# Performance work log

Measured on AMD Instinct MI355X. Metric: run time of the kernel, lower is better.

The kernel has to match this reference:

```python
import jax, jax.numpy as jnp
import numpy as np

D_EMB = 1024
D_HEAD = 64
B = 4
T = 4096


def setup_inputs() -> dict:
    key = jax.random.key(0)
    kx, kk, kq, kv = jax.random.split(key, 4)
    s = 1.0 / np.sqrt(D_EMB)  # torch Linear default init scale (uniform bound)
    x = jax.random.normal(kx, (B, T, D_EMB), dtype=jnp.float32)
    Wk = jax.random.uniform(kk, (D_HEAD, D_EMB), jnp.float32, -s, s)
    Wq = jax.random.uniform(kq, (D_HEAD, D_EMB), jnp.float32, -s, s)
    Wv = jax.random.uniform(kv, (D_HEAD, D_EMB), jnp.float32, -s, s)
    return {"x": x, "Wk": Wk, "Wq": Wq, "Wv": Wv}


def reference(x, Wk, Wq, Wv):
    # x: (B, T, d_emb); W*: (d_head, d_emb) -- torch Linear stores (out, in)
    k = jnp.einsum('bte,he->bth', x, Wk)
    q = jnp.einsum('bte,he->bth', x, Wq)
    v = jnp.einsum('bte,he->bth', x, Wv)
    scale = D_HEAD ** (-0.5)
    a = jnp.einsum('bth,bsh->bts', q, k) * scale  # (B, T, T)
    Tlen = x.shape[-2]
    causal = jnp.tril(jnp.ones((Tlen, Tlen), dtype=bool))
    a = jnp.where(causal, a, -jnp.inf)
    a = jax.nn.softmax(a, axis=-1)
    return jnp.einsum('bts,bsh->bth', a, v)  # (B, T, d_head)
```

## Files before the change

### kernel.cpp

```cpp
#include <hip/hip_runtime.h>
#include <hip/hip_bf16.h>

#define D_EMB 1024
#define T_LEN 4096
#define NTASK 576

typedef short short8 __attribute__((ext_vector_type(8)));
typedef float f32x4 __attribute__((ext_vector_type(4)));
typedef float f32x16 __attribute__((ext_vector_type(16)));
typedef float float4v __attribute__((ext_vector_type(4)));

__device__ __forceinline__ unsigned short f32_to_bf16(float f) {
    union { float f; unsigned int u; } c; c.f = f;
    unsigned int u = c.u;
    return (unsigned short)((u + 0x7FFFu + ((u >> 16) & 1u)) >> 16);
}
__device__ __forceinline__ float bf16_to_f32(unsigned short v) {
    union { unsigned int u; float f; } c; c.u = ((unsigned int)v) << 16;
    return c.f;
}
__device__ __forceinline__ unsigned cvtpk_bf16(float a, float b) {
    unsigned r;
    asm("v_cvt_pk_bf16_f32 %0, %1, %2" : "=v"(r) : "v"(a), "v"(b));
    return r;
}
__device__ __forceinline__ void gl_lds16(const void* g, void* l) {
    __builtin_amdgcn_global_load_lds(
        (const __attribute__((address_space(1))) unsigned int*)(g),
        (__attribute__((address_space(3))) unsigned int*)(l), 16, 0, 0);
}

#define QSCALE (0.125f * 1.44269504f)

__global__ __launch_bounds__(256) void convert_w(const float* __restrict__ Wk,
                                                 const float* __restrict__ Wq,
                                                 const float* __restrict__ Wv,
                                                 unsigned short* __restrict__ Wb) {
    int e = (blockIdx.x * 256 + threadIdx.x) * 8;
    const float* src;
    if (e < 65536) src = Wk + e;
    else if (e < 131072) src = Wq + (e - 65536);
    else src = Wv + (e - 131072);
    float4v a0 = *(const float4v*)src;
    float4v a1 = *(const float4v*)(src + 4);
    short8 r;
    r[0] = (short)f32_to_bf16(a0[0]); r[1] = (short)f32_to_bf16(a0[1]);
    r[2] = (short)f32_to_bf16(a0[2]); r[3] = (short)f32_to_bf16(a0[3]);
    r[4] = (short)f32_to_bf16(a1[0]); r[5] = (short)f32_to_bf16(a1[1]);
    r[6] = (short)f32_to_bf16(a1[2]); r[7] = (short)f32_to_bf16(a1[3]);
    int row = e >> 10;
    int dst = e ^ ((row & 7) << 3);
    *(short8*)(Wb + dst) = r;
}

__global__ __launch_bounds__(256, 2) void qkv_proj(const float* __restrict__ x,
                                                   const unsigned short* __restrict__ Wb,
                                                   unsigned short* __restrict__ Kb,
                                                   unsigned short* __restrict__ Qb,
                                                   unsigned short* __restrict__ Vt) {
    __shared__ __attribute__((aligned(16))) unsigned short Wsl[2][12288];

    int tid = threadIdx.x;
    int lane = tid & 63, wave = tid >> 6;
    int lo = lane & 15, hi = lane >> 4;
    int rg = wave >> 1, nh = wave & 1;
    int row0 = blockIdx.x * 32;

    const float* xp = x + (size_t)(row0 + rg * 16 + lo) * D_EMB + hi * 8;

    f32x4 acc[6];
#pragma unroll
    for (int i = 0; i < 6; i++) acc[i] = (f32x4){0.f, 0.f, 0.f, 0.f};

    float4v xa0 = *(const float4v*)(xp);
    float4v xa1 = *(const float4v*)(xp + 4);
    float4v xa2 = *(const float4v*)(xp + 32);
    float4v xa3 = *(const float4v*)(xp + 36);

#pragma unroll
    for (int j = 0; j < 6; j++) {
        int unit = j * 4 + wave;
        int u = unit * 64 + lane;
        gl_lds16(Wb + (size_t)(u >> 3) * D_EMB + (u & 7) * 8, &Wsl[0][unit * 512]);
    }
    __syncthreads();

    int buf = 0;
    int xorm = (lo & 7) << 4;
    int rowbase = nh * 96 + lo;

    for (int kt = 0; kt < 16; kt++) {
        int ktn = (kt < 15) ? kt + 1 : 15;
        const float* pn = xp + ktn * 64;
        float4v xn0 = *(const float4v*)(pn);
        float4v xn1 = *(const float4v*)(pn + 4);
        float4v xn2 = *(const float4v*)(pn + 32);
        float4v xn3 = *(const float4v*)(pn + 36);

        if (kt < 15) {
            int k0n = (kt + 1) * 64;
#pragma unroll
            for (int j = 0; j < 6; j++) {
                int unit = j * 4 + wave;
                int u = unit * 64 + lane;
                gl_lds16(Wb + (size_t)(u >> 3) * D_EMB + k0n + (u & 7) * 8,
                         &Wsl[buf ^ 1][unit * 512]);
            }
        }

        short8 af[2];
        {
            union { unsigned u[4]; short8 s; } c;
            c.u[0] = cvtpk_bf16(xa0[0], xa0[1]);
            c.u[1] = cvtpk_bf16(xa0[2], xa0[3]);
            c.u[2] = cvtpk_bf16(xa1[0], xa1[1]);
            c.u[3] = cvtpk_bf16(xa1[2], xa1[3]);
            af[0] = c.s;
            c.u[0] = cvtpk_bf16(xa2[0], xa2[1]);
            c.u[1] = cvtpk_bf16(xa2[2], xa2[3]);
            c.u[2] = cvtpk_bf16(xa3[0], xa3[1]);
            c.u[3] = cvtpk_bf16(xa3[2], xa3[3]);
            af[1] = c.s;
        }

        const char* sb = (const char*)&Wsl[buf][0];
#pragma unroll
        for (int i = 0; i < 6; i++) {
            int row = rowbase + i * 16;
#pragma unroll
            for (int ks = 0; ks < 2; ks++) {
                short8 bfrag = *(const short8*)(sb + row * 128 + ((ks * 64 + hi * 16) ^ xorm));
                acc[i] = __builtin_amdgcn_mfma_f32_16x16x32_bf16(af[ks], bfrag, acc[i], 0, 0, 0);
            }
        }
        __syncthreads();
        buf ^= 1;
        xa0 = xn0; xa1 = xn1; xa2 = xn2; xa3 = xn3;
    }

#pragma unroll
    for (int i = 0; i < 6; i++) {
        int n = nh * 6 + i;
#pragma unroll
        for (int r = 0; r < 4; r++) {
            int grow = row0 + rg * 16 + hi * 4 + r;
            float val = acc[i][r];
            if (n < 4) {
                Kb[(size_t)grow * 64 + n * 16 + lo] = f32_to_bf16(val);
            } else if (n < 8) {
                Qb[(size_t)grow * 64 + (n - 4) * 16 + lo] = f32_to_bf16(val * QSCALE);
            } else {
                int bb = grow >> 12;
                Vt[((size_t)bb * 64 + (n - 8) * 16 + lo) * T_LEN + (grow & 4095)] = f32_to_bf16(val);
            }
        }
    }
}

__global__ __launch_bounds__(64, 3) void attn(const unsigned short* __restrict__ Qb,
                                              const unsigned short* __restrict__ Kb,
                                              const unsigned short* __restrict__ Vt,
                                              unsigned short* __restrict__ Opart,
                                              float* __restrict__ Mpart,
                                              float* __restrict__ Lpart) {
    int lane = threadIdx.x;
    int q32 = lane & 31;
    int hi = lane >> 5;
    int s = blockIdx.x;
    int b = blockIdx.y;

    int k = 7, rem = s;
    while (rem >= 16 * (k + 1)) { rem -= 16 * (k + 1); k--; }
    int cpt = k + 1;
    int ti = rem / cpt;
    int t = (k << 4) + 15 - ti;
    int c = rem - ti * cpt;

    int u0 = c * 16;
    int u1 = min(u0 + 16, t + 1);

    size_t base = (size_t)b * T_LEN;
    int q0 = t * 32;
    int qg = q0 + q32;

    short8 qf[4];
    const unsigned short* qp = Qb + (base + qg) * 64 + hi * 8;
#pragma unroll
    for (int d = 0; d < 4; d++) qf[d] = *(const short8*)(qp + d * 16);

    size_t vbase = ((size_t)b * 64 + q32) * T_LEN;
    f32x16 o0 = {0.f}, o1 = {0.f};
    float m = -3e38f, l = 0.f;

    short8 kc0, kc1, kc2, kc3, vc0, vc1, vc2, vc3;
    {
        const unsigned short* kp = Kb + (base + u0 * 32 + q32) * 64 + hi * 8;
        kc0 = *(const short8*)kp;
        kc1 = *(const short8*)(kp + 16);
        kc2 = *(const short8*)(kp + 32);
        kc3 = *(const short8*)(kp + 48);
        const unsigned short* vp = Vt + vbase + u0 * 32 + hi * 8;
        vc0 = *(const short8*)vp;
        vc1 = *(const short8*)(vp + 16);
        vc2 = *(const short8*)(vp + 32 * T_LEN);
        vc3 = *(const short8*)(vp + 32 * T_LEN + 16);
    }

    for (int u = u0; u < u1; ++u) {
        int un = (u + 1 < u1) ? u + 1 : u;
        const unsigned short* kpn = Kb + (base + un * 32 + q32) * 64 + hi * 8;
        short8 kn0 = *(const short8*)kpn;
        short8 kn1 = *(const short8*)(kpn + 16);
        short8 kn2 = *(const short8*)(kpn + 32);
        short8 kn3 = *(const short8*)(kpn + 48);
        const unsigned short* vpn = Vt + vbase + un * 32 + hi * 8;
        short8 vn0 = *(const short8*)vpn;
        short8 vn1 = *(const short8*)(vpn + 16);
        short8 vn2 = *(const short8*)(vpn + 32 * T_LEN);
        short8 vn3 = *(const short8*)(vpn + 32 * T_LEN + 16);

        f32x16 sc = {0.f};
        sc = __builtin_amdgcn_mfma_f32_32x32x16_bf16(kc0, qf[0], sc, 0, 0, 0);
        sc = __builtin_amdgcn_mfma_f32_32x32x16_bf16(kc1, qf[1], sc, 0, 0, 0);
        sc = __builtin_amdgcn_mfma_f32_32x32x16_bf16(kc2, qf[2], sc, 0, 0, 0);
        sc = __builtin_amdgcn_mfma_f32_32x32x16_bf16(kc3, qf[3], sc, 0, 0, 0);

        if (u == t) {
#pragma unroll
            for (int r = 0; r < 16; ++r) {
                int ko = (r & 3) + 8 * (r >> 2) + 4 * hi;
                sc[r] = (ko <= q32) ? sc[r] : -3e38f;
            }
        }

        float x0 = fmaxf(sc[0], sc[8]),  x1 = fmaxf(sc[1], sc[9]);
        float x2 = fmaxf(sc[2], sc[10]), x3 = fmaxf(sc[3], sc[11]);
        float x4 = fmaxf(sc[4], sc[12]), x5 = fmaxf(sc[5], sc[13]);
        float x6 = fmaxf(sc[6], sc[14]), x7 = fmaxf(sc[7], sc[15]);
        x0 = fmaxf(x0, x4); x1 = fmaxf(x1, x5); x2 = fmaxf(x2, x6); x3 = fmaxf(x3, x7);
        x0 = fmaxf(x0, x2); x1 = fmaxf(x1, x3);
        float mx = fmaxf(x0, x1);
        mx = fmaxf(mx, __shfl_xor(mx, 32));

        if (__any(mx > m + 8.0f)) {
            float mn = fmaxf(m, mx);
            float al = exp2f(m - mn);
            m = mn; l *= al;
#pragma unroll
            for (int r = 0; r < 16; ++r) { o0[r] *= al; o1[r] *= al; }
        }

#pragma unroll
        for (int r = 0; r < 16; ++r) sc[r] = exp2f(sc[r] - m);
        float y0 = (sc[0] + sc[8]) + (sc[4] + sc[12]);
        float y1 = (sc[1] + sc[9]) + (sc[5] + sc[13]);
        float y2 = (sc[2] + sc[10]) + (sc[6] + sc[14]);
        float y3 = (sc[3] + sc[11]) + (sc[7] + sc[15]);
        float sum = (y0 + y1) + (y2 + y3);
        sum += __shfl_xor(sum, 32);
        l += sum;

        unsigned bb0, bb1, bb2, bb3, bb4, bb5, bb6, bb7;
        asm("v_cvt_pk_bf16_f32 %0, %1, %2" : "=v"(bb0) : "v"(sc[0]),  "v"(sc[1]));
        asm("v_cvt_pk_bf16_f32 %0, %1, %2" : "=v"(bb1) : "v"(sc[2]),  "v"(sc[3]));
        asm("v_cvt_pk_bf16_f32 %0, %1, %2" : "=v"(bb2) : "v"(sc[4]),  "v"(sc[5]));
        asm("v_cvt_pk_bf16_f32 %0, %1, %2" : "=v"(bb3) : "v"(sc[6]),  "v"(sc[7]));
        asm("v_cvt_pk_bf16_f32 %0, %1, %2" : "=v"(bb4) : "v"(sc[8]),  "v"(sc[9]));
        asm("v_cvt_pk_bf16_f32 %0, %1, %2" : "=v"(bb5) : "v"(sc[10]), "v"(sc[11]));
        asm("v_cvt_pk_bf16_f32 %0, %1, %2" : "=v"(bb6) : "v"(sc[12]), "v"(sc[13]));
        asm("v_cvt_pk_bf16_f32 %0, %1, %2" : "=v"(bb7) : "v"(sc[14]), "v"(sc[15]));
        asm("v_permlane32_swap_b32 %0, %1" : "+v"(bb0), "+v"(bb2));
        asm("v_permlane32_swap_b32 %0, %1" : "+v"(bb1), "+v"(bb3));
        asm("v_permlane32_swap_b32 %0, %1" : "+v"(bb4), "+v"(bb6));
        asm("v_permlane32_swap_b32 %0, %1" : "+v"(bb5), "+v"(bb7));
        union U8 { unsigned u[4]; short8 s; };
        U8 p0; p0.u[0] = bb0; p0.u[1] = bb1; p0.u[2] = bb2; p0.u[3] = bb3;
        U8 p1; p1.u[0] = bb4; p1.u[1] = bb5; p1.u[2] = bb6; p1.u[3] = bb7;

        o0 = __builtin_amdgcn_mfma_f32_32x32x16_bf16(vc0, p0.s, o0, 0, 0, 0);
        o0 = __builtin_amdgcn_mfma_f32_32x32x16_bf16(vc1, p1.s, o0, 0, 0, 0);
        o1 = __builtin_amdgcn_mfma_f32_32x32x16_bf16(vc2, p0.s, o1, 0, 0, 0);
        o1 = __builtin_amdgcn_mfma_f32_32x32x16_bf16(vc3, p1.s, o1, 0, 0, 0);

        kc0 = kn0; kc1 = kn1; kc2 = kn2; kc3 = kn3;
        vc0 = vn0; vc1 = vn1; vc2 = vn2; vc3 = vn3;
    }

    size_t tbase = ((size_t)(b * NTASK + s) * 32 + q32) * 64;
#pragma unroll
    for (int hb = 0; hb < 2; hb++) {
#pragma unroll
        for (int g = 0; g < 4; g++) {
            float e0 = hb ? o1[4 * g] : o0[4 * g];
            float e1 = hb ? o1[4 * g + 1] : o0[4 * g + 1];
            float e2 = hb ? o1[4 * g + 2] : o0[4 * g + 2];
            float e3 = hb ? o1[4 * g + 3] : o0[4 * g + 3];
            unsigned w0, w1;
            asm("v_cvt_pk_bf16_f32 %0, %1, %2" : "=v"(w0) : "v"(e0), "v"(e1));
            asm("v_cvt_pk_bf16_f32 %0, %1, %2" : "=v"(w1) : "v"(e2), "v"(e3));
            int h0 = hb * 32 + g * 8 + hi * 4;
            *reinterpret_cast<uint2*>(Opart + tbase + h0) = make_uint2(w0, w1);
        }
    }
    if (lane < 32) {
        Mpart[(b * NTASK + s) * 32 + q32] = m;
        Lpart[(b * NTASK + s) * 32 + q32] = l;
    }
}

__global__ __launch_bounds__(256) void attn_merge(const unsigned short* __restrict__ Opart,
                                                  const float* __restrict__ Mpart,
                                                  const float* __restrict__ Lpart,
                                                  float* __restrict__ out) {
    int tid = threadIdx.x;
    int g = blockIdx.x * 64 + (tid >> 2);
    int h0 = (tid & 3) * 16;
    int b = g >> 12, t = g & 4095;
    int tile = t >> 5, r32 = t & 31;
    int k = tile >> 4;
    int nch = k + 1;
    int s0 = 16 * (36 - (((k + 1) * (k + 2)) >> 1)) + (15 - (tile & 15)) * nch;
    int tb = b * NTASK + s0;

    float mm = -3e38f;
    for (int i = 0; i < nch; i++) mm = fmaxf(mm, Mpart[(tb + i) * 32 + r32]);
    float ll = 0.f;
    float acc[16];
#pragma unroll
    for (int e = 0; e < 16; e++) acc[e] = 0.f;
    for (int i = 0; i < nch; i++) {
        float a = exp2f(Mpart[(tb + i) * 32 + r32] - mm);
        ll += a * Lpart[(tb + i) * 32 + r32];
        const unsigned short* op = Opart + ((size_t)(tb + i) * 32 + r32) * 64 + h0;
        short8 v0 = *(const short8*)op;
        short8 v1 = *(const short8*)(op + 8);
#pragma unroll
        for (int e = 0; e < 8; e++) {
            acc[e]     += a * bf16_to_f32((unsigned short)v0[e]);
            acc[8 + e] += a * bf16_to_f32((unsigned short)v1[e]);
        }
    }
    float inv = 1.f / ll;
    float* dst = out + (size_t)g * 64 + h0;
#pragma unroll
    for (int e = 0; e < 16; e++) dst[e] = acc[e] * inv;
}

extern "C" void kernel_launch(void* const* d_in, const int* in_sizes, int n_in,
                              void* d_out, int out_size, void* d_ws, size_t ws_size,
                              hipStream_t stream) {
    (void)in_sizes; (void)n_in; (void)out_size; (void)ws_size;
    const float* x  = (const float*)d_in[0];
    const float* Wk = (const float*)d_in[1];
    const float* Wq = (const float*)d_in[2];
    const float* Wv = (const float*)d_in[3];
    float* out = (float*)d_out;

    unsigned short* Wb = (unsigned short*)d_ws;
    unsigned short* Kb = Wb + 196608;
    unsigned short* Qb = Kb + 1048576;
    unsigned short* Vt = Qb + 1048576;
    unsigned short* Opart = Vt + 1048576;
    float* Mpart = (float*)(Opart + (size_t)4 * NTASK * 32 * 64);
    float* Lpart = Mpart + 4 * NTASK * 32;

    hipLaunchKernelGGL(convert_w, dim3(96), dim3(256), 0, stream, Wk, Wq, Wv, Wb);
    hipLaunchKernelGGL(qkv_proj, dim3(512), dim3(256), 0, stream, x, Wb, Kb, Qb, Vt);
    hipLaunchKernelGGL(attn, dim3(NTASK, 4), dim3(64), 0, stream, Qb, Kb, Vt, Opart, Mpart, Lpart);
    hipLaunchKernelGGL(attn_merge, dim3(256), dim3(256), 0, stream, Opart, Mpart, Lpart, out);
}
```

Before: 83.80 us.

## Halve attention chunk size and software-pipeline QK^T one step ahead

The causal split-K attention tasks now cover 8 key tiles instead of 16, which nearly doubles the task count (NTASK 576 to 1088) and gives finer load balance and more parallelism. The merge kernel's index math is updated to match. Inside the attention loop, the QK^T MFMAs for the next key tile are issued before the current tile's softmax and PV step, with K and V loads staggered, so matrix work overlaps with softmax. The projection kernel prefetches x two k-steps ahead. The cost is more partial outputs to write and merge, plus higher register pressure.

```diff
diff --git a/kernel.cpp b/kernel.cpp
--- a/kernel.cpp
+++ b/kernel.cpp
@@ -3,7 +3,7 @@
 
 #define D_EMB 1024
 #define T_LEN 4096
-#define NTASK 576
+#define NTASK 1088
 
 typedef short short8 __attribute__((ext_vector_type(8)));
 typedef float f32x4 __attribute__((ext_vector_type(4)));
@@ -76,6 +76,10 @@
     float4v xa1 = *(const float4v*)(xp + 4);
     float4v xa2 = *(const float4v*)(xp + 32);
     float4v xa3 = *(const float4v*)(xp + 36);
+    float4v xb0 = *(const float4v*)(xp + 64);
+    float4v xb1 = *(const float4v*)(xp + 68);
+    float4v xb2 = *(const float4v*)(xp + 96);
+    float4v xb3 = *(const float4v*)(xp + 100);
 
 #pragma unroll
     for (int j = 0; j < 6; j++) {
@@ -90,12 +94,12 @@
     int rowbase = nh * 96 + lo;
 
     for (int kt = 0; kt < 16; kt++) {
-        int ktn = (kt < 15) ? kt + 1 : 15;
+        int ktn = (kt < 14) ? kt + 2 : 15;
         const float* pn = xp + ktn * 64;
-        float4v xn0 = *(const float4v*)(pn);
-        float4v xn1 = *(const float4v*)(pn + 4);
-        float4v xn2 = *(const float4v*)(pn + 32);
-        float4v xn3 = *(const float4v*)(pn + 36);
+        float4v xc0 = *(const float4v*)(pn);
+        float4v xc1 = *(const float4v*)(pn + 4);
+        float4v xc2 = *(const float4v*)(pn + 32);
+        float4v xc3 = *(const float4v*)(pn + 36);
 
         if (kt < 15) {
             int k0n = (kt + 1) * 64;
@@ -135,7 +139,8 @@
         }
         __syncthreads();
         buf ^= 1;
-        xa0 = xn0; xa1 = xn1; xa2 = xn2; xa3 = xn3;
+        xa0 = xb0; xa1 = xb1; xa2 = xb2; xa3 = xb3;
+        xb0 = xc0; xb1 = xc1; xb2 = xc2; xb3 = xc3;
     }
 
 #pragma unroll
@@ -169,19 +174,18 @@
     int s = blockIdx.x;
     int b = blockIdx.y;
 
-    int k = 7, rem = s;
-    while (rem >= 16 * (k + 1)) { rem -= 16 * (k + 1); k--; }
+    int k = 15, rem = s;
+    while (rem >= 8 * (k + 1)) { rem -= 8 * (k + 1); k--; }
     int cpt = k + 1;
     int ti = rem / cpt;
-    int t = (k << 4) + 15 - ti;
+    int t = (k << 3) + 7 - ti;
     int c = rem - ti * cpt;
 
-    int u0 = c * 16;
-    int u1 = min(u0 + 16, t + 1);
+    int u0 = c * 8;
+    int u1 = min(u0 + 8, t + 1);
 
     size_t base = (size_t)b * T_LEN;
-    int q0 = t * 32;
-    int qg = q0 + q32;
+    int qg = t * 32 + q32;
 
     short8 qf[4];
     const unsigned short* qp = Qb + (base + qg) * 64 + hi * 8;
@@ -192,51 +196,61 @@
     f32x16 o0 = {0.f}, o1 = {0.f};
     float m = -3e38f, l = 0.f;
 
-    short8 kc0, kc1, kc2, kc3, vc0, vc1, vc2, vc3;
+    short8 kB0, kB1, kB2, kB3, vA0, vA1, vA2, vA3;
     {
         const unsigned short* kp = Kb + (base + u0 * 32 + q32) * 64 + hi * 8;
-        kc0 = *(const short8*)kp;
-        kc1 = *(const short8*)(kp + 16);
-        kc2 = *(const short8*)(kp + 32);
-        kc3 = *(const short8*)(kp + 48);
+        kB0 = *(const short8*)kp;
+        kB1 = *(const short8*)(kp + 16);
+        kB2 = *(const short8*)(kp + 32);
+        kB3 = *(const short8*)(kp + 48);
+    }
+    f32x16 scC = {0.f};
+    scC = __builtin_amdgcn_mfma_f32_32x32x16_bf16(kB0, qf[0], scC, 0, 0, 0);
+    scC = __builtin_amdgcn_mfma_f32_32x32x16_bf16(kB1, qf[1], scC, 0, 0, 0);
+    scC = __builtin_amdgcn_mfma_f32_32x32x16_bf16(kB2, qf[2], scC, 0, 0, 0);
+    scC = __builtin_amdgcn_mfma_f32_32x32x16_bf16(kB3, qf[3], scC, 0, 0, 0);
+    {
         const unsigned short* vp = Vt + vbase + u0 * 32 + hi * 8;
-        vc0 = *(const short8*)vp;
-        vc1 = *(const short8*)(vp + 16);
-        vc2 = *(const short8*)(vp + 32 * T_LEN);
-        vc3 = *(const short8*)(vp + 32 * T_LEN + 16);
+        vA0 = *(const short8*)vp;
+        vA1 = *(const short8*)(vp + 16);
+        vA2 = *(const short8*)(vp + 32 * T_LEN);
+        vA3 = *(const short8*)(vp + 32 * T_LEN + 16);
+        int un = (u0 + 1 < u1) ? u0 + 1 : u0;
+        const unsigned short* kp = Kb + (base + un * 32 + q32) * 64 + hi * 8;
+        kB0 = *(const short8*)kp;
+        kB1 = *(const short8*)(kp + 16);
+        kB2 = *(const short8*)(kp + 32);
+        kB3 = *(const short8*)(kp + 48);
     }
 
     for (int u = u0; u < u1; ++u) {
-        int un = (u + 1 < u1) ? u + 1 : u;
-        const unsigned short* kpn = Kb + (base + un * 32 + q32) * 64 + hi * 8;
-        short8 kn0 = *(const short8*)kpn;
-        short8 kn1 = *(const short8*)(kpn + 16);
-        short8 kn2 = *(const short8*)(kpn + 32);
-        short8 kn3 = *(const short8*)(kpn + 48);
-        const unsigned short* vpn = Vt + vbase + un * 32 + hi * 8;
-        short8 vn0 = *(const short8*)vpn;
-        short8 vn1 = *(const short8*)(vpn + 16);
-        short8 vn2 = *(const short8*)(vpn + 32 * T_LEN);
-        short8 vn3 = *(const short8*)(vpn + 32 * T_LEN + 16);
-
-        f32x16 sc = {0.f};
-        sc = __builtin_amdgcn_mfma_f32_32x32x16_bf16(kc0, qf[0], sc, 0, 0, 0);
-        sc = __builtin_amdgcn_mfma_f32_32x32x16_bf16(kc1, qf[1], sc, 0, 0, 0);
-        sc = __builtin_amdgcn_mfma_f32_32x32x16_bf16(kc2, qf[2], sc, 0, 0, 0);
-        sc = __builtin_amdgcn_mfma_f32_32x32x16_bf16(kc3, qf[3], sc, 0, 0, 0);
+        bool hn = (u + 1 < u1);
+        f32x16 scN = {0.f};
+        if (hn) {
+            scN = __builtin_amdgcn_mfma_f32_32x32x16_bf16(kB0, qf[0], scN, 0, 0, 0);
+            scN = __builtin_amdgcn_mfma_f32_32x32x16_bf16(kB1, qf[1], scN, 0, 0, 0);
+            scN = __builtin_amdgcn_mfma_f32_32x32x16_bf16(kB2, qf[2], scN, 0, 0, 0);
+            scN = __builtin_amdgcn_mfma_f32_32x32x16_bf16(kB3, qf[3], scN, 0, 0, 0);
+            int unn = (u + 2 < u1) ? u + 2 : u + 1;
+            const unsigned short* kp = Kb + (base + unn * 32 + q32) * 64 + hi * 8;
+            kB0 = *(const short8*)kp;
+            kB1 = *(const short8*)(kp + 16);
+            kB2 = *(const short8*)(kp + 32);
+            kB3 = *(const short8*)(kp + 48);
+        }
 
         if (u == t) {
 #pragma unroll
             for (int r = 0; r < 16; ++r) {
                 int ko = (r & 3) + 8 * (r >> 2) + 4 * hi;
-                sc[r] = (ko <= q32) ? sc[r] : -3e38f;
+                scC[r] = (ko <= q32) ? scC[r] : -3e38f;
             }
         }
 
-        float x0 = fmaxf(sc[0], sc[8]),  x1 = fmaxf(sc[1], sc[9]);
-        float x2 = fmaxf(sc[2], sc[10]), x3 = fmaxf(sc[3], sc[11]);
-        float x4 = fmaxf(sc[4], sc[12]), x5 = fmaxf(sc[5], sc[13]);
-        float x6 = fmaxf(sc[6], sc[14]), x7 = fmaxf(sc[7], sc[15]);
+        float x0 = fmaxf(scC[0], scC[8]),  x1 = fmaxf(scC[1], scC[9]);
+        float x2 = fmaxf(scC[2], scC[10]), x3 = fmaxf(scC[3], scC[11]);
+        float x4 = fmaxf(scC[4], scC[12]), x5 = fmaxf(scC[5], scC[13]);
+        float x6 = fmaxf(scC[6], scC[14]), x7 = fmaxf(scC[7], scC[15]);
         x0 = fmaxf(x0, x4); x1 = fmaxf(x1, x5); x2 = fmaxf(x2, x6); x3 = fmaxf(x3, x7);
         x0 = fmaxf(x0, x2); x1 = fmaxf(x1, x3);
         float mx = fmaxf(x0, x1);
@@ -251,24 +265,24 @@
         }
 
 #pragma unroll
-        for (int r = 0; r < 16; ++r) sc[r] = exp2f(sc[r] - m);
-        float y0 = (sc[0] + sc[8]) + (sc[4] + sc[12]);
-        float y1 = (sc[1] + sc[9]) + (sc[5] + sc[13]);
-        float y2 = (sc[2] + sc[10]) + (sc[6] + sc[14]);
-        float y3 = (sc[3] + sc[11]) + (sc[7] + sc[15]);
+        for (int r = 0; r < 16; ++r) scC[r] = exp2f(scC[r] - m);
+        float y0 = (scC[0] + scC[8]) + (scC[4] + scC[12]);
+        float y1 = (scC[1] + scC[9]) + (scC[5] + scC[13]);
+        float y2 = (scC[2] + scC[10]) + (scC[6] + scC[14]);
+        float y3 = (scC[3] + scC[11]) + (scC[7] + scC[15]);
         float sum = (y0 + y1) + (y2 + y3);
         sum += __shfl_xor(sum, 32);
         l += sum;
 
         unsigned bb0, bb1, bb2, bb3, bb4, bb5, bb6, bb7;
-        asm("v_cvt_pk_bf16_f32 %0, %1, %2" : "=v"(bb0) : "v"(sc[0]),  "v"(sc[1]));
-        asm("v_cvt_pk_bf16_f32 %0, %1, %2" : "=v"(bb1) : "v"(sc[2]),  "v"(sc[3]));
-        asm("v_cvt_pk_bf16_f32 %0, %1, %2" : "=v"(bb2) : "v"(sc[4]),  "v"(sc[5]));
-        asm("v_cvt_pk_bf16_f32 %0, %1, %2" : "=v"(bb3) : "v"(sc[6]),  "v"(sc[7]));
-        asm("v_cvt_pk_bf16_f32 %0, %1, %2" : "=v"(bb4) : "v"(sc[8]),  "v"(sc[9]));
-        asm("v_cvt_pk_bf16_f32 %0, %1, %2" : "=v"(bb5) : "v"(sc[10]), "v"(sc[11]));
-        asm("v_cvt_pk_bf16_f32 %0, %1, %2" : "=v"(bb6) : "v"(sc[12]), "v"(sc[13]));
-        asm("v_cvt_pk_bf16_f32 %0, %1, %2" : "=v"(bb7) : "v"(sc[14]), "v"(sc[15]));
+        bb0 = cvtpk_bf16(scC[0],  scC[1]);
+        bb1 = cvtpk_bf16(scC[2],  scC[3]);
+        bb2 = cvtpk_bf16(scC[4],  scC[5]);
+        bb3 = cvtpk_bf16(scC[6],  scC[7]);
+        bb4 = cvtpk_bf16(scC[8],  scC[9]);
+        bb5 = cvtpk_bf16(scC[10], scC[11]);
+        bb6 = cvtpk_bf16(scC[12], scC[13]);
+        bb7 = cvtpk_bf16(scC[14], scC[15]);
         asm("v_permlane32_swap_b32 %0, %1" : "+v"(bb0), "+v"(bb2));
         asm("v_permlane32_swap_b32 %0, %1" : "+v"(bb1), "+v"(bb3));
         asm("v_permlane32_swap_b32 %0, %1" : "+v"(bb4), "+v"(bb6));
@@ -277,13 +291,19 @@
         U8 p0; p0.u[0] = bb0; p0.u[1] = bb1; p0.u[2] = bb2; p0.u[3] = bb3;
         U8 p1; p1.u[0] = bb4; p1.u[1] = bb5; p1.u[2] = bb6; p1.u[3] = bb7;
 
-        o0 = __builtin_amdgcn_mfma_f32_32x32x16_bf16(vc0, p0.s, o0, 0, 0, 0);
-        o0 = __builtin_amdgcn_mfma_f32_32x32x16_bf16(vc1, p1.s, o0, 0, 0, 0);
-        o1 = __builtin_amdgcn_mfma_f32_32x32x16_bf16(vc2, p0.s, o1, 0, 0, 0);
-        o1 = __builtin_amdgcn_mfma_f32_32x32x16_bf16(vc3, p1.s, o1, 0, 0, 0);
-
-        kc0 = kn0; kc1 = kn1; kc2 = kn2; kc3 = kn3;
-        vc0 = vn0; vc1 = vn1; vc2 = vn2; vc3 = vn3;
+        o0 = __builtin_amdgcn_mfma_f32_32x32x16_bf16(vA0, p0.s, o0, 0, 0, 0);
+        o0 = __builtin_amdgcn_mfma_f32_32x32x16_bf16(vA1, p1.s, o0, 0, 0, 0);
+        o1 = __builtin_amdgcn_mfma_f32_32x32x16_bf16(vA2, p0.s, o1, 0, 0, 0);
+        o1 = __builtin_amdgcn_mfma_f32_32x32x16_bf16(vA3, p1.s, o1, 0, 0, 0);
+
+        if (hn) {
+            const unsigned short* vp = Vt + vbase + (u + 1) * 32 + hi * 8;
+            vA0 = *(const short8*)vp;
+            vA1 = *(const short8*)(vp + 16);
+            vA2 = *(const short8*)(vp + 32 * T_LEN);
+            vA3 = *(const short8*)(vp + 32 * T_LEN + 16);
+        }
+        scC = scN;
     }
 
     size_t tbase = ((size_t)(b * NTASK + s) * 32 + q32) * 64;
@@ -295,9 +315,8 @@
             float e1 = hb ? o1[4 * g + 1] : o0[4 * g + 1];
             float e2 = hb ? o1[4 * g + 2] : o0[4 * g + 2];
             float e3 = hb ? o1[4 * g + 3] : o0[4 * g + 3];
-            unsigned w0, w1;
-            asm("v_cvt_pk_bf16_f32 %0, %1, %2" : "=v"(w0) : "v"(e0), "v"(e1));
-            asm("v_cvt_pk_bf16_f32 %0, %1, %2" : "=v"(w1) : "v"(e2), "v"(e3));
+            unsigned w0 = cvtpk_bf16(e0, e1);
+            unsigned w1 = cvtpk_bf16(e2, e3);
             int h0 = hb * 32 + g * 8 + hi * 4;
             *reinterpret_cast<uint2*>(Opart + tbase + h0) = make_uint2(w0, w1);
         }
@@ -317,9 +336,9 @@
     int h0 = (tid & 3) * 16;
     int b = g >> 12, t = g & 4095;
     int tile = t >> 5, r32 = t & 31;
-    int k = tile >> 4;
+    int k = tile >> 3;
     int nch = k + 1;
-    int s0 = 16 * (36 - (((k + 1) * (k + 2)) >> 1)) + (15 - (tile & 15)) * nch;
+    int s0 = 8 * (136 - (((k + 1) * (k + 2)) >> 1)) + (7 - (tile & 7)) * nch;
     int tb = b * NTASK + s0;
 
     float mm = -3e38f;
```

After: 93.92 us. 1.12x slower.

## Halve attention split-K chunk size, interleave batch in grid, deepen x prefetch

Applied to the files above, without the earlier changes.

The attention work split changes from 16-tile to 8-tile key chunks. That roughly doubles the task count (1088 per batch), and the merge kernel's indexing is updated to match. The grid is flattened to 1D with the batch index in the low bits so neighbouring blocks span batches. Occupancy is raised from 3 to 4 waves per launch bound, and the K/V register prefetch in the attention loop is dropped. The projection kernel prefetches x two k-steps ahead instead of one. Together these aim to improve load balance and latency hiding, at the cost of more partial outputs to write and merge and less in-loop prefetching.

```diff
diff --git a/kernel.cpp b/kernel.cpp
--- a/kernel.cpp
+++ b/kernel.cpp
@@ -3,7 +3,7 @@
 
 #define D_EMB 1024
 #define T_LEN 4096
-#define NTASK 576
+#define NTASK 1088
 
 typedef short short8 __attribute__((ext_vector_type(8)));
 typedef float f32x4 __attribute__((ext_vector_type(4)));
@@ -76,6 +76,10 @@
     float4v xa1 = *(const float4v*)(xp + 4);
     float4v xa2 = *(const float4v*)(xp + 32);
     float4v xa3 = *(const float4v*)(xp + 36);
+    float4v xb0 = *(const float4v*)(xp + 64);
+    float4v xb1 = *(const float4v*)(xp + 68);
+    float4v xb2 = *(const float4v*)(xp + 96);
+    float4v xb3 = *(const float4v*)(xp + 100);
 
 #pragma unroll
     for (int j = 0; j < 6; j++) {
@@ -90,12 +94,12 @@
     int rowbase = nh * 96 + lo;
 
     for (int kt = 0; kt < 16; kt++) {
-        int ktn = (kt < 15) ? kt + 1 : 15;
+        int ktn = (kt < 14) ? kt + 2 : 15;
         const float* pn = xp + ktn * 64;
-        float4v xn0 = *(const float4v*)(pn);
-        float4v xn1 = *(const float4v*)(pn + 4);
-        float4v xn2 = *(const float4v*)(pn + 32);
-        float4v xn3 = *(const float4v*)(pn + 36);
+        float4v xc0 = *(const float4v*)(pn);
+        float4v xc1 = *(const float4v*)(pn + 4);
+        float4v xc2 = *(const float4v*)(pn + 32);
+        float4v xc3 = *(const float4v*)(pn + 36);
 
         if (kt < 15) {
             int k0n = (kt + 1) * 64;
@@ -135,7 +139,8 @@
         }
         __syncthreads();
         buf ^= 1;
-        xa0 = xn0; xa1 = xn1; xa2 = xn2; xa3 = xn3;
+        xa0 = xb0; xa1 = xb1; xa2 = xb2; xa3 = xb3;
+        xb0 = xc0; xb1 = xc1; xb2 = xc2; xb3 = xc3;
     }
 
 #pragma unroll
@@ -157,7 +162,7 @@
     }
 }
 
-__global__ __launch_bounds__(64, 3) void attn(const unsigned short* __restrict__ Qb,
+__global__ __launch_bounds__(64, 4) void attn(const unsigned short* __restrict__ Qb,
                                               const unsigned short* __restrict__ Kb,
                                               const unsigned short* __restrict__ Vt,
                                               unsigned short* __restrict__ Opart,
@@ -166,22 +171,22 @@
     int lane = threadIdx.x;
     int q32 = lane & 31;
     int hi = lane >> 5;
-    int s = blockIdx.x;
-    int b = blockIdx.y;
-
-    int k = 7, rem = s;
-    while (rem >= 16 * (k + 1)) { rem -= 16 * (k + 1); k--; }
+    unsigned lin = blockIdx.x;
+    int b = lin & 3;
+    int s = (int)(((lin >> 3) << 1) | ((lin >> 2) & 1));
+
+    int k = 15, rem = s;
+    while (rem >= 8 * (k + 1)) { rem -= 8 * (k + 1); k--; }
     int cpt = k + 1;
     int ti = rem / cpt;
-    int t = (k << 4) + 15 - ti;
+    int t = (k << 3) + 7 - ti;
     int c = rem - ti * cpt;
 
-    int u0 = c * 16;
-    int u1 = min(u0 + 16, t + 1);
+    int u0 = c * 8;
+    int u1 = min(u0 + 8, t + 1);
 
     size_t base = (size_t)b * T_LEN;
-    int q0 = t * 32;
-    int qg = q0 + q32;
+    int qg = t * 32 + q32;
 
     short8 qf[4];
     const unsigned short* qp = Qb + (base + qg) * 64 + hi * 8;
@@ -192,32 +197,17 @@
     f32x16 o0 = {0.f}, o1 = {0.f};
     float m = -3e38f, l = 0.f;
 
-    short8 kc0, kc1, kc2, kc3, vc0, vc1, vc2, vc3;
-    {
-        const unsigned short* kp = Kb + (base + u0 * 32 + q32) * 64 + hi * 8;
-        kc0 = *(const short8*)kp;
-        kc1 = *(const short8*)(kp + 16);
-        kc2 = *(const short8*)(kp + 32);
-        kc3 = *(const short8*)(kp + 48);
-        const unsigned short* vp = Vt + vbase + u0 * 32 + hi * 8;
-        vc0 = *(const short8*)vp;
-        vc1 = *(const short8*)(vp + 16);
-        vc2 = *(const short8*)(vp + 32 * T_LEN);
-        vc3 = *(const short8*)(vp + 32 * T_LEN + 16);
-    }
-
     for (int u = u0; u < u1; ++u) {
-        int un = (u + 1 < u1) ? u + 1 : u;
-        const unsigned short* kpn = Kb + (base + un * 32 + q32) * 64 + hi * 8;
-        short8 kn0 = *(const short8*)kpn;
-        short8 kn1 = *(const short8*)(kpn + 16);
-        short8 kn2 = *(const short8*)(kpn + 32);
-        short8 kn3 = *(const short8*)(kpn + 48);
-        const unsigned short* vpn = Vt + vbase + un * 32 + hi * 8;
-        short8 vn0 = *(const short8*)vpn;
-        short8 vn1 = *(const short8*)(vpn + 16);
-        short8 vn2 = *(const short8*)(vpn + 32 * T_LEN);
-        short8 vn3 = *(const short8*)(vpn + 32 * T_LEN + 16);
+        const unsigned short* kp = Kb + (base + u * 32 + q32) * 64 + hi * 8;
+        short8 kc0 = *(const short8*)kp;
+        short8 kc1 = *(const short8*)(kp + 16);
+        short8 kc2 = *(const short8*)(kp + 32);
+        short8 kc3 = *(const short8*)(kp + 48);
+        const unsigned short* vp = Vt + vbase + u * 32 + hi * 8;
+        short8 vc0 = *(const short8*)vp;
+        short8 vc1 = *(const short8*)(vp + 16);
+        short8 vc2 = *(const short8*)(vp + 32 * T_LEN);
+        short8 vc3 = *(const short8*)(vp + 32 * T_LEN + 16);
 
         f32x16 sc = {0.f};
         sc = __builtin_amdgcn_mfma_f32_32x32x16_bf16(kc0, qf[0], sc, 0, 0, 0);
@@ -233,13 +223,14 @@
             }
         }
 
-        float x0 = fmaxf(sc[0], sc[8]),  x1 = fmaxf(sc[1], sc[9]);
-        float x2 = fmaxf(sc[2], sc[10]), x3 = fmaxf(sc[3], sc[11]);
-        float x4 = fmaxf(sc[4], sc[12]), x5 = fmaxf(sc[5], sc[13]);
-        float x6 = fmaxf(sc[6], sc[14]), x7 = fmaxf(sc[7], sc[15]);
-        x0 = fmaxf(x0, x4); x1 = fmaxf(x1, x5); x2 = fmaxf(x2, x6); x3 = fmaxf(x3, x7);
-        x0 = fmaxf(x0, x2); x1 = fmaxf(x1, x3);
-        float mx = fmaxf(x0, x1);
+        float t0 = fmaxf(fmaxf(sc[0], sc[1]), sc[2]);
+        float t1 = fmaxf(fmaxf(sc[3], sc[4]), sc[5]);
+        float t2 = fmaxf(fmaxf(sc[6], sc[7]), sc[8]);
+        float t3 = fmaxf(fmaxf(sc[9], sc[10]), sc[11]);
+        float t4 = fmaxf(fmaxf(sc[12], sc[13]), sc[14]);
+        float t5 = fmaxf(fmaxf(t0, t1), sc[15]);
+        float t6 = fmaxf(fmaxf(t2, t3), t4);
+        float mx = fmaxf(t5, t6);
         mx = fmaxf(mx, __shfl_xor(mx, 32));
 
         if (__any(mx > m + 8.0f)) {
@@ -261,14 +252,14 @@
         l += sum;
 
         unsigned bb0, bb1, bb2, bb3, bb4, bb5, bb6, bb7;
-        asm("v_cvt_pk_bf16_f32 %0, %1, %2" : "=v"(bb0) : "v"(sc[0]),  "v"(sc[1]));
-        asm("v_cvt_pk_bf16_f32 %0, %1, %2" : "=v"(bb1) : "v"(sc[2]),  "v"(sc[3]));
-        asm("v_cvt_pk_bf16_f32 %0, %1, %2" : "=v"(bb2) : "v"(sc[4]),  "v"(sc[5]));
-        asm("v_cvt_pk_bf16_f32 %0, %1, %2" : "=v"(bb3) : "v"(sc[6]),  "v"(sc[7]));
-        asm("v_cvt_pk_bf16_f32 %0, %1, %2" : "=v"(bb4) : "v"(sc[8]),  "v"(sc[9]));
-        asm("v_cvt_pk_bf16_f32 %0, %1, %2" : "=v"(bb5) : "v"(sc[10]), "v"(sc[11]));
-        asm("v_cvt_pk_bf16_f32 %0, %1, %2" : "=v"(bb6) : "v"(sc[12]), "v"(sc[13]));
-        asm("v_cvt_pk_bf16_f32 %0, %1, %2" : "=v"(bb7) : "v"(sc[14]), "v"(sc[15]));
+        bb0 = cvtpk_bf16(sc[0],  sc[1]);
+        bb1 = cvtpk_bf16(sc[2],  sc[3]);
+        bb2 = cvtpk_bf16(sc[4],  sc[5]);
+        bb3 = cvtpk_bf16(sc[6],  sc[7]);
+        bb4 = cvtpk_bf16(sc[8],  sc[9]);
+        bb5 = cvtpk_bf16(sc[10], sc[11]);
+        bb6 = cvtpk_bf16(sc[12], sc[13]);
+        bb7 = cvtpk_bf16(sc[14], sc[15]);
         asm("v_permlane32_swap_b32 %0, %1" : "+v"(bb0), "+v"(bb2));
         asm("v_permlane32_swap_b32 %0, %1" : "+v"(bb1), "+v"(bb3));
         asm("v_permlane32_swap_b32 %0, %1" : "+v"(bb4), "+v"(bb6));
@@ -281,9 +272,6 @@
         o0 = __builtin_amdgcn_mfma_f32_32x32x16_bf16(vc1, p1.s, o0, 0, 0, 0);
         o1 = __builtin_amdgcn_mfma_f32_32x32x16_bf16(vc2, p0.s, o1, 0, 0, 0);
         o1 = __builtin_amdgcn_mfma_f32_32x32x16_bf16(vc3, p1.s, o1, 0, 0, 0);
-
-        kc0 = kn0; kc1 = kn1; kc2 = kn2; kc3 = kn3;
-        vc0 = vn0; vc1 = vn1; vc2 = vn2; vc3 = vn3;
     }
 
     size_t tbase = ((size_t)(b * NTASK + s) * 32 + q32) * 64;
@@ -295,9 +283,8 @@
             float e1 = hb ? o1[4 * g + 1] : o0[4 * g + 1];
             float e2 = hb ? o1[4 * g + 2] : o0[4 * g + 2];
             float e3 = hb ? o1[4 * g + 3] : o0[4 * g + 3];
-            unsigned w0, w1;
-            asm("v_cvt_pk_bf16_f32 %0, %1, %2" : "=v"(w0) : "v"(e0), "v"(e1));
-            asm("v_cvt_pk_bf16_f32 %0, %1, %2" : "=v"(w1) : "v"(e2), "v"(e3));
+            unsigned w0 = cvtpk_bf16(e0, e1);
+            unsigned w1 = cvtpk_bf16(e2, e3);
             int h0 = hb * 32 + g * 8 + hi * 4;
             *reinterpret_cast<uint2*>(Opart + tbase + h0) = make_uint2(w0, w1);
         }
@@ -317,9 +304,9 @@
     int h0 = (tid & 3) * 16;
     int b = g >> 12, t = g & 4095;
     int tile = t >> 5, r32 = t & 31;
-    int k = tile >> 4;
+    int k = tile >> 3;
     int nch = k + 1;
-    int s0 = 16 * (36 - (((k + 1) * (k + 2)) >> 1)) + (15 - (tile & 15)) * nch;
+    int s0 = 8 * (136 - (((k + 1) * (k + 2)) >> 1)) + (7 - (tile & 7)) * nch;
     int tb = b * NTASK + s0;
 
     float mm = -3e38f;
@@ -366,6 +353,6 @@
 
     hipLaunchKernelGGL(convert_w, dim3(96), dim3(256), 0, stream, Wk, Wq, Wv, Wb);
     hipLaunchKernelGGL(qkv_proj, dim3(512), dim3(256), 0, stream, x, Wb, Kb, Qb, Vt);
-    hipLaunchKernelGGL(attn, dim3(NTASK, 4), dim3(64), 0, stream, Qb, Kb, Vt, Opart, Mpart, Lpart);
+    hipLaunchKernelGGL(attn, dim3(4 * NTASK), dim3(64), 0, stream, Qb, Kb, Vt, Opart, Mpart, Lpart);
     hipLaunchKernelGGL(attn_merge, dim3(256), dim3(256), 0, stream, Opart, Mpart, Lpart, out);
 }
```

Result: slower. 93.14 us (+11.1%).
